# Kernel tuning notes

Hardware: AMD Instinct MI355X
Metric: run time of the kernel (lower is better)

## Reference

```python
import jax, jax.numpy as jnp
import numpy as np

N = 100_000   # nodes
E = 3_200_000 # edges
G = 128       # graphs in batch
H = 32        # hidden_dim
PI = float(np.pi)


def setup_inputs() -> dict:
    key = jax.random.key(0)
    ks = jax.random.split(key, 18)
    p = lambda k, s: (jax.random.normal(k, s, dtype=jnp.float32) * 0.1)
    x = jax.random.normal(ks[0], (N, 1), dtype=jnp.float32)
    edge_index = jax.random.randint(ks[1], (2, E), 0, N, dtype=jnp.int32)
    batch = jnp.sort(jax.random.randint(ks[2], (N,), 0, G, dtype=jnp.int32))
    return dict(
        x=x, edge_index=edge_index, batch=batch,
        W1=p(ks[3], (1, H)),  b1=jnp.zeros((H,), jnp.float32),
        W2=p(ks[4], (H, H)),  b2=jnp.zeros((H,), jnp.float32),
        W3=p(ks[5], (H, H)),  b3=jnp.zeros((H,), jnp.float32),
        Wt1=p(ks[6], (H, 32)), bt1=jnp.zeros((32,), jnp.float32),
        Wt2=p(ks[7], (32, 1)), bt2=jnp.zeros((1,), jnp.float32),
        Wg1=p(ks[8], (H, 32)), bg1=jnp.zeros((32,), jnp.float32),
        Wg2=p(ks[9], (32, 2)), bg2=jnp.zeros((2,), jnp.float32),
    )


def _gcn_norm(edge_index):
    # PyG GCNConv default: add self-loops, symmetric normalization.
    loop = jnp.arange(N, dtype=edge_index.dtype)
    src = jnp.concatenate([edge_index[0], loop])
    dst = jnp.concatenate([edge_index[1], loop])
    deg = jax.ops.segment_sum(jnp.ones_like(dst, dtype=jnp.float32), dst, num_segments=N)
    dinv = jnp.where(deg > 0, jax.lax.rsqrt(jnp.maximum(deg, 1.0)), 0.0)
    norm = dinv[src] * dinv[dst]  # [E+N]
    return src, dst, norm


def _gcn_conv(x, W, b, src, dst, norm):
    h = x @ W                                  # [N, out]
    msg = h[src] * norm[:, None]               # gather + scale  [E+N, out]
    return jax.ops.segment_sum(msg, dst, num_segments=N) + b


def _forward(x, W1, b1, W2, b2, W3, b3, Wt1, bt1, Wt2, bt2, Wg1, bg1, Wg2, bg2,
             edge_index, batch):
    src, dst, norm = _gcn_norm(edge_index)
    x = jax.nn.relu(_gcn_conv(x, W1, b1, src, dst, norm))
    x = jax.nn.relu(_gcn_conv(x, W2, b2, src, dst, norm))
    h = jax.nn.relu(_gcn_conv(x, W3, b3, src, dst, norm))
    # theta head per node
    theta = PI * jax.nn.sigmoid(jax.nn.relu(h @ Wt1 + bt1) @ Wt2 + bt2)[:, 0]  # [N]
    # global mean pool per graph
    counts = jax.ops.segment_sum(jnp.ones((N,), jnp.float32), batch, num_segments=G)
    gsum = jax.ops.segment_sum(h, batch, num_segments=G)
    gemb = gsum / jnp.maximum(counts, 1.0)[:, None]                            # [G, H]
    beta_gamma = 2.0 * PI * jax.nn.sigmoid(jax.nn.relu(gemb @ Wg1 + bg1) @ Wg2 + bg2)  # [G, 2]
    return theta, beta_gamma


def reference(x, edge_index, batch, W1, b1, W2, b2, W3, b3,
              Wt1, bt1, Wt2, bt2, Wg1, bg1, Wg2, bg2):
    return _forward(x, W1, b1, W2, b2, W3, b3, Wt1, bt1, Wt2, bt2,
                    Wg1, bg1, Wg2, bg2, edge_index, batch)
```

## Files before the change

### kernel.cpp

```cpp
#include <hip/hip_runtime.h>
#include <hip/hip_bf16.h>

#define PI_F 3.14159265358979323846f
#define NBLK 256
#define BSH 8
#define BSZ 256
#define SCAP 10240

static inline size_t align256(size_t x) { return (x + 255) & ~size_t(255); }

__device__ __forceinline__ float bflo(unsigned w) { return __uint_as_float(w << 16); }
__device__ __forceinline__ float bfhi(unsigned w) { return __uint_as_float(w & 0xFFFF0000u); }
__device__ __forceinline__ unsigned bfpack(float a, float b) {
    unsigned lo = (__float_as_uint(a) + 0x8000u) >> 16;
    unsigned hi = (__float_as_uint(b) + 0x8000u) & 0xFFFF0000u;
    return lo | hi;
}

#define BF_ACC8(base, q) \
    acc[(base)+0] += bflo((q).x); acc[(base)+1] += bfhi((q).x); \
    acc[(base)+2] += bflo((q).y); acc[(base)+3] += bfhi((q).y); \
    acc[(base)+4] += bflo((q).z); acc[(base)+5] += bfhi((q).z); \
    acc[(base)+6] += bflo((q).w); acc[(base)+7] += bfhi((q).w);


__global__ void __launch_bounds__(1024) count_kernel(
                             const int* __restrict__ dst, int* __restrict__ C,
                             int E, int CHUNK, int NB2) {
    extern __shared__ int hist[];
    for (int i = threadIdx.x; i < NB2; i += 1024) hist[i] = 0;
    __syncthreads();
    int s0 = blockIdx.x * CHUNK, s1 = min(s0 + CHUNK, E);
    for (int e = s0 + threadIdx.x; e < s1; e += 1024)
        atomicAdd(&hist[dst[e] >> BSH], 1);
    __syncthreads();
    for (int i = threadIdx.x; i < NB2; i += 1024)
        C[(size_t)blockIdx.x * NB2 + i] = hist[i];
}

__global__ void scan_blocks_kernel(int* __restrict__ C, int* __restrict__ colsum, int NB2) {
    __shared__ int s[256];
    int k = blockIdx.x;
    int b = threadIdx.x;
    int v = C[(size_t)b * NB2 + k];
    s[b] = v;
    __syncthreads();
    for (int off = 1; off < 256; off <<= 1) {
        int w = (b >= off) ? s[b - off] : 0;
        __syncthreads();
        s[b] += w;
        __syncthreads();
    }
    C[(size_t)b * NB2 + k] = s[b] - v;
    if (b == 255) colsum[k] = s[255];
}

__global__ void scan_totals_kernel(const int* __restrict__ colsum, int* __restrict__ bbase,
                                   int NB2, int E) {
    __shared__ int s[256];
    __shared__ int running;
    if (threadIdx.x == 0) running = 0;
    __syncthreads();
    for (int base = 0; base < NB2; base += 256) {
        int i = base + threadIdx.x;
        int v = (i < NB2) ? colsum[i] : 0;
        s[threadIdx.x] = v;
        __syncthreads();
        for (int off = 1; off < 256; off <<= 1) {
            int w = (threadIdx.x >= (unsigned)off) ? s[threadIdx.x - off] : 0;
            __syncthreads();
            s[threadIdx.x] += w;
            __syncthreads();
        }
        if (i < NB2) bbase[i] = running + s[threadIdx.x] - v;
        __syncthreads();
        if (threadIdx.x == 255) running += s[255];
        __syncthreads();
    }
    if (threadIdx.x == 0) bbase[NB2] = E;
}

__global__ void __launch_bounds__(1024) scatter_kernel(
                               const int* __restrict__ src, const int* __restrict__ dst,
                               const int* __restrict__ C, const int* __restrict__ bbase,
                               unsigned* __restrict__ bkt_data, int E, int CHUNK, int NB2) {
    extern __shared__ int ofs[];
    for (int i = threadIdx.x; i < NB2; i += 1024)
        ofs[i] = bbase[i] + C[(size_t)blockIdx.x * NB2 + i];
    __syncthreads();
    int s0 = blockIdx.x * CHUNK, s1 = min(s0 + CHUNK, E);
    for (int e = s0 + threadIdx.x; e < s1; e += 1024) {
        int d = dst[e];
        int p = atomicAdd(&ofs[d >> BSH], 1);
        bkt_data[p] = ((unsigned)(d & (BSZ - 1)) << 17) | (unsigned)src[e];
    }
}

__global__ void __launch_bounds__(512) csr_build_kernel(
                                 const unsigned* __restrict__ bkt_data, const int* __restrict__ bbase,
                                 const float* __restrict__ x,
                                 unsigned* __restrict__ csr, int* __restrict__ e_start,
                                 float* __restrict__ dinv, float* __restrict__ xd,
                                 int N, int NB2) {
    __shared__ unsigned sdata[SCAP];
    __shared__ int hist[256];
    __shared__ int scn[256];
    __shared__ int bump[256];
    int tid = threadIdx.x;
    int b = blockIdx.x;
    int g0 = bbase[b], g1 = bbase[b + 1];
    int cnt = g1 - g0;
    bool fits = (cnt <= SCAP);
    if (tid < 256) hist[tid] = 0;
    __syncthreads();
    for (int i = tid; i < cnt; i += 512) {
        unsigned pk = bkt_data[g0 + i];
        if (fits) sdata[i] = pk;
        atomicAdd(&hist[pk >> 17], 1);
    }
    __syncthreads();
    int orig = (tid < 256) ? hist[tid] : 0;
    if (tid < 256) scn[tid] = orig;
    __syncthreads();
    for (int off = 1; off < 256; off <<= 1) {
        int w = (tid >= off && tid < 256) ? scn[tid - off] : 0;
        __syncthreads();
        if (tid < 256) scn[tid] += w;
        __syncthreads();
    }
    if (tid < 256) {
        int excl = scn[tid] - orig;
        bump[tid] = g0 + excl;
        int node = b * BSZ + tid;
        if (node < N) {
            float dv = rsqrtf((float)(orig + 1));
            dinv[node] = dv;
            xd[node] = x[node] * dv;
            e_start[node] = g0 + excl;
        }
    }
    if (b == NB2 - 1 && tid == 0) e_start[N] = g1;
    __syncthreads();
    for (int i = tid; i < cnt; i += 512) {
        unsigned pk = fits ? sdata[i] : bkt_data[g0 + i];
        int p = atomicAdd(&bump[pk >> 17], 1);
        csr[p] = pk & 0x1FFFFu;
    }
}


__global__ void __launch_bounds__(256) agg1_kernel(
                            const float* __restrict__ xd, const int* __restrict__ e_start,
                            const unsigned* __restrict__ csr, const float* __restrict__ dinv,
                            const float* __restrict__ W1, const float* __restrict__ b1,
                            const float* __restrict__ W2,
                            unsigned short* __restrict__ ub, int n) {
    __shared__ float sW2[1024];
    __shared__ float sW1[32], sb1[32];
    for (int i = threadIdx.x; i < 1024; i += 256) sW2[i] = W2[i];
    if (threadIdx.x < 32) { sW1[threadIdx.x] = W1[threadIdx.x]; sb1[threadIdx.x] = b1[threadIdx.x]; }
    __syncthreads();
    int d = blockIdx.x * 256 + threadIdx.x;
    if (d >= n) return;
    int e0 = e_start[d];
    int cnt = e_start[d + 1] - e0;
    float s = 0.f;
    int j = 0;
    for (; j + 4 <= cnt; j += 4) {
        int s0 = (int)csr[e0 + j], s1 = (int)csr[e0 + j + 1];
        int s2 = (int)csr[e0 + j + 2], s3 = (int)csr[e0 + j + 3];
        s += xd[s0]; s += xd[s1]; s += xd[s2]; s += xd[s3];
    }
    for (; j < cnt; j++) s += xd[(int)csr[e0 + j]];
    float dv = dinv[d];
    float tt = dv * (s + xd[d]);
    float h1[32];
#pragma unroll
    for (int f = 0; f < 32; f++) h1[f] = fmaxf(tt * sW1[f] + sb1[f], 0.f);
    float o[32];
#pragma unroll
    for (int f = 0; f < 32; f++) o[f] = 0.f;
#pragma unroll
    for (int k = 0; k < 32; k++) {
        float vk = h1[k];
#pragma unroll
        for (int fq = 0; fq < 8; fq++) {
            float4 w4 = *(const float4*)(sW2 + k * 32 + fq * 4);
            o[fq * 4 + 0] += vk * w4.x; o[fq * 4 + 1] += vk * w4.y;
            o[fq * 4 + 2] += vk * w4.z; o[fq * 4 + 3] += vk * w4.w;
        }
    }
    unsigned ow[16];
#pragma unroll
    for (int i2 = 0; i2 < 16; i2++) ow[i2] = bfpack(dv * o[2 * i2], dv * o[2 * i2 + 1]);
    uint4* dstp = (uint4*)(ub + ((size_t)d << 5));
    dstp[0] = *(uint4*)&ow[0];  dstp[1] = *(uint4*)&ow[4];
    dstp[2] = *(uint4*)&ow[8];  dstp[3] = *(uint4*)&ow[12];
}

__device__ __forceinline__ void row_gather(const unsigned short* __restrict__ ub,
                                           const unsigned* __restrict__ csr,
                                           int e0, int cnt, int d, float* acc) {
#pragma unroll
    for (int f = 0; f < 32; f++) acc[f] = 0.f;
    int j = 0;
    for (; j + 2 <= cnt; j += 2) {
        int s0 = (int)csr[e0 + j], s1 = (int)csr[e0 + j + 1];
        const uint4* r0 = (const uint4*)(ub + ((size_t)s0 << 5));
        const uint4* r1 = (const uint4*)(ub + ((size_t)s1 << 5));
        uint4 q0 = r0[0], q1 = r0[1], q2 = r0[2], q3 = r0[3];
        uint4 p0 = r1[0], p1 = r1[1], p2 = r1[2], p3 = r1[3];
        BF_ACC8(0, q0); BF_ACC8(8, q1); BF_ACC8(16, q2); BF_ACC8(24, q3);
        BF_ACC8(0, p0); BF_ACC8(8, p1); BF_ACC8(16, p2); BF_ACC8(24, p3);
    }
    if (j < cnt) {
        int s0 = (int)csr[e0 + j];
        const uint4* r0 = (const uint4*)(ub + ((size_t)s0 << 5));
        uint4 q0 = r0[0], q1 = r0[1], q2 = r0[2], q3 = r0[3];
        BF_ACC8(0, q0); BF_ACC8(8, q1); BF_ACC8(16, q2); BF_ACC8(24, q3);
    }
    const uint4* rs = (const uint4*)(ub + ((size_t)d << 5));
    uint4 q0 = rs[0], q1 = rs[1], q2 = rs[2], q3 = rs[3];
    BF_ACC8(0, q0); BF_ACC8(8, q1); BF_ACC8(16, q2); BF_ACC8(24, q3);
}

__global__ void __launch_bounds__(256, 2) agg2_kernel(
                            const unsigned short* __restrict__ ub,
                            const int* __restrict__ e_start, const unsigned* __restrict__ csr,
                            const float* __restrict__ dinv, const float* __restrict__ bias,
                            const float* __restrict__ W,
                            unsigned short* __restrict__ ob, int n) {
    __shared__ float sW[1024];
    __shared__ float sb[32];
    for (int i = threadIdx.x; i < 1024; i += 256) sW[i] = W[i];
    if (threadIdx.x < 32) sb[threadIdx.x] = bias[threadIdx.x];
    __syncthreads();
    int d = blockIdx.x * 256 + threadIdx.x;
    if (d >= n) return;
    int e0 = e_start[d];
    int cnt = e_start[d + 1] - e0;
    float acc[32];
    row_gather(ub, csr, e0, cnt, d, acc);
    float dv = dinv[d];
#pragma unroll
    for (int f = 0; f < 32; f++) acc[f] = fmaxf(dv * acc[f] + sb[f], 0.f);
    float o[32];
#pragma unroll
    for (int f = 0; f < 32; f++) o[f] = 0.f;
#pragma unroll
    for (int k = 0; k < 32; k++) {
        float vk = acc[k];
#pragma unroll
        for (int fq = 0; fq < 8; fq++) {
            float4 w4 = *(const float4*)(sW + k * 32 + fq * 4);
            o[fq * 4 + 0] += vk * w4.x; o[fq * 4 + 1] += vk * w4.y;
            o[fq * 4 + 2] += vk * w4.z; o[fq * 4 + 3] += vk * w4.w;
        }
    }
    unsigned ow[16];
#pragma unroll
    for (int i2 = 0; i2 < 16; i2++) ow[i2] = bfpack(dv * o[2 * i2], dv * o[2 * i2 + 1]);
    uint4* dstp = (uint4*)(ob + ((size_t)d << 5));
    dstp[0] = *(uint4*)&ow[0];  dstp[1] = *(uint4*)&ow[4];
    dstp[2] = *(uint4*)&ow[8];  dstp[3] = *(uint4*)&ow[12];
}

__global__ void __launch_bounds__(256, 2) agg3_kernel(
                            const unsigned short* __restrict__ ub,
                            const int* __restrict__ e_start, const unsigned* __restrict__ csr,
                            const float* __restrict__ dinv, const float* __restrict__ bias,
                            const float* __restrict__ Wt1, const float* __restrict__ bt1,
                            const float* __restrict__ Wt2, const float* __restrict__ bt2,
                            unsigned short* __restrict__ hb, float* __restrict__ theta, int n) {
    __shared__ float sW[1024];
    __shared__ float sb[32], sbt[32], sw2[32];
    for (int i = threadIdx.x; i < 1024; i += 256) sW[i] = Wt1[i];
    if (threadIdx.x < 32) {
        sb[threadIdx.x] = bias[threadIdx.x];
        sbt[threadIdx.x] = bt1[threadIdx.x];
        sw2[threadIdx.x] = Wt2[threadIdx.x];
    }
    __syncthreads();
    int d = blockIdx.x * 256 + threadIdx.x;
    if (d >= n) return;
    int e0 = e_start[d];
    int cnt = e_start[d + 1] - e0;
    float acc[32];
    row_gather(ub, csr, e0, cnt, d, acc);
    float dv = dinv[d];
#pragma unroll
    for (int f = 0; f < 32; f++) acc[f] = fmaxf(dv * acc[f] + sb[f], 0.f);
    unsigned ow[16];
#pragma unroll
    for (int i2 = 0; i2 < 16; i2++) ow[i2] = bfpack(acc[2 * i2], acc[2 * i2 + 1]);
    uint4* dstp = (uint4*)(hb + ((size_t)d << 5));
    dstp[0] = *(uint4*)&ow[0];  dstp[1] = *(uint4*)&ow[4];
    dstp[2] = *(uint4*)&ow[8];  dstp[3] = *(uint4*)&ow[12];
    float o[32];
#pragma unroll
    for (int f = 0; f < 32; f++) o[f] = 0.f;
#pragma unroll
    for (int k = 0; k < 32; k++) {
        float vk = acc[k];
#pragma unroll
        for (int fq = 0; fq < 8; fq++) {
            float4 w4 = *(const float4*)(sW + k * 32 + fq * 4);
            o[fq * 4 + 0] += vk * w4.x; o[fq * 4 + 1] += vk * w4.y;
            o[fq * 4 + 2] += vk * w4.z; o[fq * 4 + 3] += vk * w4.w;
        }
    }
    float tl = 0.f;
#pragma unroll
    for (int f = 0; f < 32; f++) tl += fmaxf(o[f] + sbt[f], 0.f) * sw2[f];
    theta[d] = PI_F / (1.f + __expf(-(tl + bt2[0])));
}


__global__ void gb_kernel(const int* __restrict__ batch, int* __restrict__ gstart,
                          int n, int G) {
    int i = blockIdx.x * 256 + threadIdx.x;
    if (i >= n) return;
    int g = batch[i];
    if (i == 0) {
        for (int gg = 0; gg <= g; gg++) gstart[gg] = 0;
    } else {
        int gp = batch[i - 1];
        for (int gg = gp + 1; gg <= g; gg++) gstart[gg] = i;
    }
    if (i == n - 1) {
        for (int gg = g + 1; gg <= G; gg++) gstart[gg] = n;
    }
}

__global__ void __launch_bounds__(512) bg_kernel(
                          const unsigned short* __restrict__ hb, const int* __restrict__ gstart,
                          const float* __restrict__ Wg1, const float* __restrict__ bg1v,
                          const float* __restrict__ Wg2, const float* __restrict__ bg2v,
                          float* __restrict__ out, int G) {
    __shared__ float sW[1024];
    __shared__ float part[8][32];
    for (int i = threadIdx.x; i < 1024; i += 512) sW[i] = Wg1[i];
    int g = blockIdx.x;
    int s = gstart[g], e = gstart[g + 1];
    int w = threadIdx.x >> 6;
    int lane = threadIdx.x & 63;
    int f = lane & 31, h = lane >> 5;
    float a = 0.f;
    for (int i = s + (w << 1) + h; i < e; i += 16)
        a += __uint_as_float((unsigned)hb[((size_t)i << 5) + f] << 16);
    a += __shfl_xor(a, 32, 64);
    if (h == 0) part[w][f] = a;
    __syncthreads();
    if (w == 0) {
        float hv = 0.f;
#pragma unroll
        for (int p = 0; p < 8; p++) hv += part[p][f];
        hv /= fmaxf((float)(e - s), 1.f);
        int base = lane & 32;
        float acc = bg1v[f];
#pragma unroll
        for (int k = 0; k < 32; k++) acc += __shfl(hv, base | k, 64) * sW[k * 32 + f];
        acc = fmaxf(acc, 0.f);
        float p0 = acc * Wg2[f * 2 + 0];
        float p1 = acc * Wg2[f * 2 + 1];
#pragma unroll
        for (int m = 1; m < 32; m <<= 1) {
            p0 += __shfl_xor(p0, m, 64);
            p1 += __shfl_xor(p1, m, 64);
        }
        if (lane == 0) {
            out[g * 2 + 0] = 2.f * PI_F / (1.f + __expf(-(p0 + bg2v[0])));
            out[g * 2 + 1] = 2.f * PI_F / (1.f + __expf(-(p1 + bg2v[1])));
        }
    }
}


extern "C" void kernel_launch(void* const* d_in, const int* in_sizes, int n_in,
                              void* d_out, int out_size, void* d_ws, size_t ws_size,
                              hipStream_t stream) {
    const float* x   = (const float*)d_in[0];
    const int*   ei  = (const int*)d_in[1];
    const int* batch = (const int*)d_in[2];
    const float* W1  = (const float*)d_in[3];
    const float* b1  = (const float*)d_in[4];
    const float* W2  = (const float*)d_in[5];
    const float* b2  = (const float*)d_in[6];
    const float* W3  = (const float*)d_in[7];
    const float* b3  = (const float*)d_in[8];
    const float* Wt1 = (const float*)d_in[9];
    const float* bt1 = (const float*)d_in[10];
    const float* Wt2 = (const float*)d_in[11];
    const float* bt2 = (const float*)d_in[12];
    const float* Wg1 = (const float*)d_in[13];
    const float* bg1 = (const float*)d_in[14];
    const float* Wg2 = (const float*)d_in[15];
    const float* bg2 = (const float*)d_in[16];

    const int N = in_sizes[0];
    const int E = in_sizes[1] / 2;
    const int G = 128;
    const int* src = ei;
    const int* dst = ei + E;
    float* theta_out = (float*)d_out;
    float* bg_out = (float*)d_out + N;

    const int NB2 = (N + BSZ - 1) >> BSH;
    const int CHUNK = (E + NBLK - 1) / NBLK;

    char* w = (char*)d_ws;
    auto alloc = [&](size_t bytes) -> char* { char* p = w; w += align256(bytes); return p; };
    int*      C        = (int*)alloc((size_t)NBLK * NB2 * 4);
    int*      colsum   = (int*)alloc((size_t)NB2 * 4);
    int*      bbase    = (int*)alloc((size_t)(NB2 + 1) * 4);
    unsigned* bkt_data = (unsigned*)alloc((size_t)E * 4);
    unsigned* csr      = (unsigned*)alloc((size_t)E * 4);
    int*      e_start  = (int*)alloc((size_t)(N + 1) * 4);
    float*    dinv     = (float*)alloc((size_t)N * 4);
    float*    xd       = (float*)alloc((size_t)N * 4);
    unsigned short* u2b = (unsigned short*)alloc((size_t)N * 64);
    unsigned short* u3b = (unsigned short*)alloc((size_t)N * 64);
    unsigned short* hb  = (unsigned short*)alloc((size_t)N * 64);
    int*      gstart   = (int*)alloc((size_t)(G + 1) * 4);

    size_t ldsB = (size_t)NB2 * 4;
    count_kernel<<<NBLK, 1024, ldsB, stream>>>(dst, C, E, CHUNK, NB2);
    scan_blocks_kernel<<<NB2, 256, 0, stream>>>(C, colsum, NB2);
    scan_totals_kernel<<<1, 256, 0, stream>>>(colsum, bbase, NB2, E);
    scatter_kernel<<<NBLK, 1024, ldsB, stream>>>(src, dst, C, bbase, bkt_data, E, CHUNK, NB2);
    csr_build_kernel<<<NB2, 512, 0, stream>>>(bkt_data, bbase, x, csr, e_start, dinv, xd, N, NB2);
    gb_kernel<<<(N + 255) / 256, 256, 0, stream>>>(batch, gstart, N, G);

    unsigned gridN = (unsigned)((N + 255) / 256);

    agg1_kernel<<<gridN, 256, 0, stream>>>(xd, e_start, csr, dinv, W1, b1, W2, u2b, N);
    agg2_kernel<<<gridN, 256, 0, stream>>>(u2b, e_start, csr, dinv, b2, W3, u3b, N);
    agg3_kernel<<<gridN, 256, 0, stream>>>(u3b, e_start, csr, dinv, b3,
                                           Wt1, bt1, Wt2, bt2, hb, theta_out, N);

    bg_kernel<<<G, 512, 0, stream>>>(hb, gstart, Wg1, bg1, Wg2, bg2, bg_out, G);
}
```

Before: 335.6 us.

## Split each node across four lanes in aggregation kernels with shuffle-based matmul

The three aggregation kernels now assign four threads per destination node. Each thread gathers one 16-byte quarter of every neighbor's bf16 feature row and owns 8 of the 32 output features, exchanging inputs for the 32x32 matmul via wavefront shuffles. The intent is to cut per-thread register pressure (32-float accumulators down to 8), raise occupancy and memory-level parallelism, and make neighbor-row loads coalesced across lanes. In exchange, CSR indices are read by four threads each, shuffle traffic is added, and the launch grid is four times larger.

```diff
diff --git a/kernel.cpp b/kernel.cpp
--- a/kernel.cpp
+++ b/kernel.cpp
@@ -17,11 +17,11 @@
     return lo | hi;
 }
 
-#define BF_ACC8(base, q) \
-    acc[(base)+0] += bflo((q).x); acc[(base)+1] += bfhi((q).x); \
-    acc[(base)+2] += bflo((q).y); acc[(base)+3] += bfhi((q).y); \
-    acc[(base)+4] += bflo((q).z); acc[(base)+5] += bfhi((q).z); \
-    acc[(base)+6] += bflo((q).w); acc[(base)+7] += bfhi((q).w);
+#define BF_ACC8Q(q) \
+    acc[0] += bflo((q).x); acc[1] += bfhi((q).x); \
+    acc[2] += bflo((q).y); acc[3] += bfhi((q).y); \
+    acc[4] += bflo((q).z); acc[5] += bfhi((q).z); \
+    acc[6] += bflo((q).w); acc[7] += bfhi((q).w);
 
 
 __global__ void __launch_bounds__(1024) count_kernel(
@@ -149,6 +149,24 @@
 }
 
 
+__device__ __forceinline__ void mm32_8(const float* __restrict__ sW, const float vr[8],
+                                       int sub, int lane, float o[8]) {
+    const float4* sW4 = (const float4*)sW;
+    int base = lane & ~3;
+#pragma unroll
+    for (int r = 0; r < 4; r++) {
+#pragma unroll
+        for (int i = 0; i < 8; i++) {
+            float vk = __shfl(vr[i], base | r, 64);
+            int k = r * 8 + i;
+            float4 w0 = sW4[k * 8 + sub * 2];
+            float4 w1 = sW4[k * 8 + sub * 2 + 1];
+            o[0] += vk * w0.x; o[1] += vk * w0.y; o[2] += vk * w0.z; o[3] += vk * w0.w;
+            o[4] += vk * w1.x; o[5] += vk * w1.y; o[6] += vk * w1.z; o[7] += vk * w1.w;
+        }
+    }
+}
+
 __global__ void __launch_bounds__(256) agg1_kernel(
                             const float* __restrict__ xd, const int* __restrict__ e_start,
                             const unsigned* __restrict__ csr, const float* __restrict__ dinv,
@@ -160,71 +178,37 @@
     for (int i = threadIdx.x; i < 1024; i += 256) sW2[i] = W2[i];
     if (threadIdx.x < 32) { sW1[threadIdx.x] = W1[threadIdx.x]; sb1[threadIdx.x] = b1[threadIdx.x]; }
     __syncthreads();
-    int d = blockIdx.x * 256 + threadIdx.x;
+    int t = blockIdx.x * 256 + threadIdx.x;
+    int d = t >> 2, sub = t & 3;
+    int lane = threadIdx.x & 63;
     if (d >= n) return;
     int e0 = e_start[d];
     int cnt = e_start[d + 1] - e0;
     float s = 0.f;
-    int j = 0;
-    for (; j + 4 <= cnt; j += 4) {
-        int s0 = (int)csr[e0 + j], s1 = (int)csr[e0 + j + 1];
-        int s2 = (int)csr[e0 + j + 2], s3 = (int)csr[e0 + j + 3];
-        s += xd[s0]; s += xd[s1]; s += xd[s2]; s += xd[s3];
-    }
-    for (; j < cnt; j++) s += xd[(int)csr[e0 + j]];
+    int j = sub;
+    for (; j + 8 <= cnt; j += 8) {
+        int i0 = (int)csr[e0 + j], i1 = (int)csr[e0 + j + 4];
+        s += xd[i0]; s += xd[i1];
+    }
+    for (; j < cnt; j += 4) s += xd[(int)csr[e0 + j]];
+    s += __shfl_xor(s, 1, 64);
+    s += __shfl_xor(s, 2, 64);
     float dv = dinv[d];
     float tt = dv * (s + xd[d]);
-    float h1[32];
-#pragma unroll
-    for (int f = 0; f < 32; f++) h1[f] = fmaxf(tt * sW1[f] + sb1[f], 0.f);
-    float o[32];
-#pragma unroll
-    for (int f = 0; f < 32; f++) o[f] = 0.f;
-#pragma unroll
-    for (int k = 0; k < 32; k++) {
-        float vk = h1[k];
-#pragma unroll
-        for (int fq = 0; fq < 8; fq++) {
-            float4 w4 = *(const float4*)(sW2 + k * 32 + fq * 4);
-            o[fq * 4 + 0] += vk * w4.x; o[fq * 4 + 1] += vk * w4.y;
-            o[fq * 4 + 2] += vk * w4.z; o[fq * 4 + 3] += vk * w4.w;
-        }
-    }
-    unsigned ow[16];
-#pragma unroll
-    for (int i2 = 0; i2 < 16; i2++) ow[i2] = bfpack(dv * o[2 * i2], dv * o[2 * i2 + 1]);
-    uint4* dstp = (uint4*)(ub + ((size_t)d << 5));
-    dstp[0] = *(uint4*)&ow[0];  dstp[1] = *(uint4*)&ow[4];
-    dstp[2] = *(uint4*)&ow[8];  dstp[3] = *(uint4*)&ow[12];
-}
-
-__device__ __forceinline__ void row_gather(const unsigned short* __restrict__ ub,
-                                           const unsigned* __restrict__ csr,
-                                           int e0, int cnt, int d, float* acc) {
-#pragma unroll
-    for (int f = 0; f < 32; f++) acc[f] = 0.f;
-    int j = 0;
-    for (; j + 2 <= cnt; j += 2) {
-        int s0 = (int)csr[e0 + j], s1 = (int)csr[e0 + j + 1];
-        const uint4* r0 = (const uint4*)(ub + ((size_t)s0 << 5));
-        const uint4* r1 = (const uint4*)(ub + ((size_t)s1 << 5));
-        uint4 q0 = r0[0], q1 = r0[1], q2 = r0[2], q3 = r0[3];
-        uint4 p0 = r1[0], p1 = r1[1], p2 = r1[2], p3 = r1[3];
-        BF_ACC8(0, q0); BF_ACC8(8, q1); BF_ACC8(16, q2); BF_ACC8(24, q3);
-        BF_ACC8(0, p0); BF_ACC8(8, p1); BF_ACC8(16, p2); BF_ACC8(24, p3);
-    }
-    if (j < cnt) {
-        int s0 = (int)csr[e0 + j];
-        const uint4* r0 = (const uint4*)(ub + ((size_t)s0 << 5));
-        uint4 q0 = r0[0], q1 = r0[1], q2 = r0[2], q3 = r0[3];
-        BF_ACC8(0, q0); BF_ACC8(8, q1); BF_ACC8(16, q2); BF_ACC8(24, q3);
-    }
-    const uint4* rs = (const uint4*)(ub + ((size_t)d << 5));
-    uint4 q0 = rs[0], q1 = rs[1], q2 = rs[2], q3 = rs[3];
-    BF_ACC8(0, q0); BF_ACC8(8, q1); BF_ACC8(16, q2); BF_ACC8(24, q3);
-}
-
-__global__ void __launch_bounds__(256, 2) agg2_kernel(
+    float vr[8];
+#pragma unroll
+    for (int i = 0; i < 8; i++) vr[i] = fmaxf(tt * sW1[sub * 8 + i] + sb1[sub * 8 + i], 0.f);
+    float o[8];
+#pragma unroll
+    for (int i = 0; i < 8; i++) o[i] = 0.f;
+    mm32_8(sW2, vr, sub, lane, o);
+    unsigned ow[4];
+#pragma unroll
+    for (int i2 = 0; i2 < 4; i2++) ow[i2] = bfpack(dv * o[2 * i2], dv * o[2 * i2 + 1]);
+    ((uint4*)ub)[(size_t)d * 4 + sub] = *(uint4*)&ow[0];
+}
+
+__global__ void __launch_bounds__(256) agg2_kernel(
                             const unsigned short* __restrict__ ub,
                             const int* __restrict__ e_start, const unsigned* __restrict__ csr,
                             const float* __restrict__ dinv, const float* __restrict__ bias,
@@ -235,37 +219,50 @@
     for (int i = threadIdx.x; i < 1024; i += 256) sW[i] = W[i];
     if (threadIdx.x < 32) sb[threadIdx.x] = bias[threadIdx.x];
     __syncthreads();
-    int d = blockIdx.x * 256 + threadIdx.x;
+    int t = blockIdx.x * 256 + threadIdx.x;
+    int d = t >> 2, sub = t & 3;
+    int lane = threadIdx.x & 63;
     if (d >= n) return;
     int e0 = e_start[d];
     int cnt = e_start[d + 1] - e0;
-    float acc[32];
-    row_gather(ub, csr, e0, cnt, d, acc);
+    float acc[8];
+#pragma unroll
+    for (int i = 0; i < 8; i++) acc[i] = 0.f;
+    const uint4* rows = (const uint4*)ub;
+    int j = 0;
+    for (; j + 4 <= cnt; j += 4) {
+        int i0 = (int)csr[e0 + j],     i1 = (int)csr[e0 + j + 1];
+        int i2 = (int)csr[e0 + j + 2], i3 = (int)csr[e0 + j + 3];
+        uint4 q0 = rows[(size_t)i0 * 4 + sub];
+        uint4 q1 = rows[(size_t)i1 * 4 + sub];
+        uint4 q2 = rows[(size_t)i2 * 4 + sub];
+        uint4 q3 = rows[(size_t)i3 * 4 + sub];
+        BF_ACC8Q(q0); BF_ACC8Q(q1); BF_ACC8Q(q2); BF_ACC8Q(q3);
+    }
+    for (; j < cnt; j++) {
+        int i0 = (int)csr[e0 + j];
+        uint4 q0 = rows[(size_t)i0 * 4 + sub];
+        BF_ACC8Q(q0);
+    }
+    {
+        uint4 q0 = rows[(size_t)d * 4 + sub];
+        BF_ACC8Q(q0);
+    }
     float dv = dinv[d];
-#pragma unroll
-    for (int f = 0; f < 32; f++) acc[f] = fmaxf(dv * acc[f] + sb[f], 0.f);
-    float o[32];
-#pragma unroll
-    for (int f = 0; f < 32; f++) o[f] = 0.f;
-#pragma unroll
-    for (int k = 0; k < 32; k++) {
-        float vk = acc[k];
-#pragma unroll
-        for (int fq = 0; fq < 8; fq++) {
-            float4 w4 = *(const float4*)(sW + k * 32 + fq * 4);
-            o[fq * 4 + 0] += vk * w4.x; o[fq * 4 + 1] += vk * w4.y;
-            o[fq * 4 + 2] += vk * w4.z; o[fq * 4 + 3] += vk * w4.w;
-        }
-    }
-    unsigned ow[16];
-#pragma unroll
-    for (int i2 = 0; i2 < 16; i2++) ow[i2] = bfpack(dv * o[2 * i2], dv * o[2 * i2 + 1]);
-    uint4* dstp = (uint4*)(ob + ((size_t)d << 5));
-    dstp[0] = *(uint4*)&ow[0];  dstp[1] = *(uint4*)&ow[4];
-    dstp[2] = *(uint4*)&ow[8];  dstp[3] = *(uint4*)&ow[12];
-}
-
-__global__ void __launch_bounds__(256, 2) agg3_kernel(
+    float vr[8];
+#pragma unroll
+    for (int i = 0; i < 8; i++) vr[i] = fmaxf(dv * acc[i] + sb[sub * 8 + i], 0.f);
+    float o[8];
+#pragma unroll
+    for (int i = 0; i < 8; i++) o[i] = 0.f;
+    mm32_8(sW, vr, sub, lane, o);
+    unsigned ow[4];
+#pragma unroll
+    for (int i2 = 0; i2 < 4; i2++) ow[i2] = bfpack(dv * o[2 * i2], dv * o[2 * i2 + 1]);
+    ((uint4*)ob)[(size_t)d * 4 + sub] = *(uint4*)&ow[0];
+}
+
+__global__ void __launch_bounds__(256) agg3_kernel(
                             const unsigned short* __restrict__ ub,
                             const int* __restrict__ e_start, const unsigned* __restrict__ csr,
                             const float* __restrict__ dinv, const float* __restrict__ bias,
@@ -281,38 +278,54 @@
         sw2[threadIdx.x] = Wt2[threadIdx.x];
     }
     __syncthreads();
-    int d = blockIdx.x * 256 + threadIdx.x;
+    int t = blockIdx.x * 256 + threadIdx.x;
+    int d = t >> 2, sub = t & 3;
+    int lane = threadIdx.x & 63;
     if (d >= n) return;
     int e0 = e_start[d];
     int cnt = e_start[d + 1] - e0;
-    float acc[32];
-    row_gather(ub, csr, e0, cnt, d, acc);
+    float acc[8];
+#pragma unroll
+    for (int i = 0; i < 8; i++) acc[i] = 0.f;
+    const uint4* rows = (const uint4*)ub;
+    int j = 0;
+    for (; j + 4 <= cnt; j += 4) {
+        int i0 = (int)csr[e0 + j],     i1 = (int)csr[e0 + j + 1];
+        int i2 = (int)csr[e0 + j + 2], i3 = (int)csr[e0 + j + 3];
+        uint4 q0 = rows[(size_t)i0 * 4 + sub];
+        uint4 q1 = rows[(size_t)i1 * 4 + sub];
+        uint4 q2 = rows[(size_t)i2 * 4 + sub];
+        uint4 q3 = rows[(size_t)i3 * 4 + sub];
+        BF_ACC8Q(q0); BF_ACC8Q(q1); BF_ACC8Q(q2); BF_ACC8Q(q3);
+    }
+    for (; j < cnt; j++) {
+        int i0 = (int)csr[e0 + j];
+        uint4 q0 = rows[(size_t)i0 * 4 + sub];
+        BF_ACC8Q(q0);
+    }
+    {
+        uint4 q0 = rows[(size_t)d * 4 + sub];
+        BF_ACC8Q(q0);
+    }
     float dv = dinv[d];
-#pragma unroll
-    for (int f = 0; f < 32; f++) acc[f] = fmaxf(dv * acc[f] + sb[f], 0.f);
-    unsigned ow[16];
-#pragma unroll
-    for (int i2 = 0; i2 < 16; i2++) ow[i2] = bfpack(acc[2 * i2], acc[2 * i2 + 1]);
-    uint4* dstp = (uint4*)(hb + ((size_t)d << 5));
-    dstp[0] = *(uint4*)&ow[0];  dstp[1] = *(uint4*)&ow[4];
-    dstp[2] = *(uint4*)&ow[8];  dstp[3] = *(uint4*)&ow[12];
-    float o[32];
-#pragma unroll
-    for (int f = 0; f < 32; f++) o[f] = 0.f;
-#pragma unroll
-    for (int k = 0; k < 32; k++) {
-        float vk = acc[k];
-#pragma unroll
-        for (int fq = 0; fq < 8; fq++) {
-            float4 w4 = *(const float4*)(sW + k * 32 + fq * 4);
-            o[fq * 4 + 0] += vk * w4.x; o[fq * 4 + 1] += vk * w4.y;
-            o[fq * 4 + 2] += vk * w4.z; o[fq * 4 + 3] += vk * w4.w;
-        }
-    }
+    float vr[8];
+#pragma unroll
+    for (int i = 0; i < 8; i++) vr[i] = fmaxf(dv * acc[i] + sb[sub * 8 + i], 0.f);
+    unsigned ow[4];
+#pragma unroll
+    for (int i2 = 0; i2 < 4; i2++) ow[i2] = bfpack(vr[2 * i2], vr[2 * i2 + 1]);
+    ((uint4*)hb)[(size_t)d * 4 + sub] = *(uint4*)&ow[0];
+    float o[8];
+#pragma unroll
+    for (int i = 0; i < 8; i++) o[i] = 0.f;
+    mm32_8(sW, vr, sub, lane, o);
     float tl = 0.f;
 #pragma unroll
-    for (int f = 0; f < 32; f++) tl += fmaxf(o[f] + sbt[f], 0.f) * sw2[f];
-    theta[d] = PI_F / (1.f + __expf(-(tl + bt2[0])));
+    for (int i = 0; i < 8; i++)
+        tl += fmaxf(o[i] + sbt[sub * 8 + i], 0.f) * sw2[sub * 8 + i];
+    tl += __shfl_xor(tl, 1, 64);
+    tl += __shfl_xor(tl, 2, 64);
+    if (sub == 0) theta[d] = PI_F / (1.f + __expf(-(tl + bt2[0])));
 }
 
 
@@ -431,11 +444,11 @@
     csr_build_kernel<<<NB2, 512, 0, stream>>>(bkt_data, bbase, x, csr, e_start, dinv, xd, N, NB2);
     gb_kernel<<<(N + 255) / 256, 256, 0, stream>>>(batch, gstart, N, G);
 
-    unsigned gridN = (unsigned)((N + 255) / 256);
-
-    agg1_kernel<<<gridN, 256, 0, stream>>>(xd, e_start, csr, dinv, W1, b1, W2, u2b, N);
-    agg2_kernel<<<gridN, 256, 0, stream>>>(u2b, e_start, csr, dinv, b2, W3, u3b, N);
-    agg3_kernel<<<gridN, 256, 0, stream>>>(u3b, e_start, csr, dinv, b3,
+    unsigned gridQ = (unsigned)(((size_t)N * 4 + 255) / 256);
+
+    agg1_kernel<<<gridQ, 256, 0, stream>>>(xd, e_start, csr, dinv, W1, b1, W2, u2b, N);
+    agg2_kernel<<<gridQ, 256, 0, stream>>>(u2b, e_start, csr, dinv, b2, W3, u3b, N);
+    agg3_kernel<<<gridQ, 256, 0, stream>>>(u3b, e_start, csr, dinv, b3,
                                            Wt1, bt1, Wt2, bt2, hb, theta_out, N);
 
     bg_kernel<<<G, 512, 0, stream>>>(hb, gstart, Wg1, bg1, Wg2, bg2, bg_out, G);
```

Measured after the change: 294.6 us. 12.2% less time.
